# Kernel optimization log

Hardware: AMD Instinct MI355X
Metric: run time of the kernel (lower is better)

Reference implementation:

```python
import jax, jax.numpy as jnp
import numpy as np

EPS = 1e-5
MODES = 64
KERNEL = 25
PRED = 336
N_ENC = 2

def rmsnorm(x, w):
    return x * jax.lax.rsqrt(jnp.mean(jnp.square(x), axis=-1, keepdims=True) + EPS) * w

def ffn(x, w1, b1, w2, b2):
    return jax.nn.gelu(x @ w1 + b1, approximate=False) @ w2 + b2

def series_decomp(x):
    # moving average with zero padding (Conv1d, kernel=KERNEL, weight=1/KERNEL)
    pad = (KERNEL - 1) // 2
    xp = jnp.pad(x, ((0, 0), (pad, pad), (0, 0)))
    cs = jnp.cumsum(xp, axis=1)
    cs = jnp.concatenate([jnp.zeros_like(cs[:, :1]), cs], axis=1)
    t = (cs[:, KERNEL:, :] - cs[:, :-KERNEL, :]) / KERNEL  # [B,T,C]
    return x - t, t

def fourier_block(x, w, nw):
    # x: [B,T,C]; w: [MODES,C,2] learned complex weights; nw: [C] rms scale
    B, T, C = x.shape
    Xf = jnp.fft.rfft(x, axis=1)                      # [B,F,C] complex64
    mag = jnp.sum(Xf[:, 1:].real**2 + Xf[:, 1:].imag**2, axis=-1)  # [B,F-1]
    K = min(MODES, Xf.shape[1] - 1)
    _, idx = jax.lax.top_k(mag, K)
    idx = idx + 1                                      # skip DC, [B,K]
    Xsel = jnp.take_along_axis(Xf, idx[:, :, None], axis=1)  # [B,K,C]
    Wc = w[:K, :, 0] + 1j * w[:K, :, 1]               # [K,C]
    Ysel = Xsel * Wc[None]                             # [B,K,C]
    Yf = jnp.zeros_like(Xf).at[jnp.arange(B)[:, None], idx].set(Ysel)
    y = jnp.fft.irfft(Yf, n=T, axis=1)                 # [B,T,C]
    return rmsnorm(y, nw)

def setup_inputs() -> dict:
    key = jax.random.key(0)
    ks = iter(jax.random.split(key, 64))
    B, L, Cin, Cout, D, FF = 32, 1024, 8, 8, 512, 2048
    r = lambda *s: jax.random.normal(next(ks), s, dtype=jnp.float32) * 0.02
    z = lambda *s: jnp.zeros(s, dtype=jnp.float32)
    o = lambda *s: jnp.ones(s, dtype=jnp.float32)
    return {
        'x': jax.random.normal(next(ks), (B, L, Cin), dtype=jnp.float32),
        'enc_in_w': r(Cin, D), 'enc_in_b': z(D),
        'dec_in_w': r(Cin, D), 'dec_in_b': z(D),
        'enc_freq_w': r(N_ENC, MODES, D, 2), 'enc_freq_nw': o(N_ENC, D),
        'enc_n1': o(N_ENC, D), 'enc_n2': o(N_ENC, D),
        'enc_w1': r(N_ENC, D, FF), 'enc_b1': z(N_ENC, FF),
        'enc_w2': r(N_ENC, FF, D), 'enc_b2': z(N_ENC, D),
        'dec_freq_w': r(MODES, D, 2), 'dec_freq_nw': o(D),
        'dec_n1': o(D), 'dec_n2': o(D), 'dec_nx': o(D),
        'dec_cross_w': r(D, D), 'dec_cross_b': z(D),
        'dec_w1': r(D, FF), 'dec_b1': z(FF),
        'dec_w2': r(FF, D), 'dec_b2': z(D),
        'seas_w': r(D, Cout), 'seas_b': z(Cout),
        'tr_w1': r(D, FF), 'tr_b1': z(FF),
        'tr_w2': r(FF, Cout), 'tr_b2': z(Cout),
        'mix_w': r(Cout, Cout), 'mix_b': z(Cout),
        'qpos': jax.random.normal(next(ks), (1, PRED, D), dtype=jnp.float32) * 0.02,
    }

def reference(x, enc_in_w, enc_in_b, dec_in_w, dec_in_b,
              enc_freq_w, enc_freq_nw, enc_n1, enc_n2, enc_w1, enc_b1, enc_w2, enc_b2,
              dec_freq_w, dec_freq_nw, dec_n1, dec_n2, dec_nx, dec_cross_w, dec_cross_b,
              dec_w1, dec_b1, dec_w2, dec_b2, seas_w, seas_b,
              tr_w1, tr_b1, tr_w2, tr_b2, mix_w, mix_b, qpos):
    s, t = series_decomp(x)
    sez = s @ enc_in_w + enc_in_b                      # [B,L,D]
    for i in range(N_ENC):
        sez = sez + fourier_block(rmsnorm(sez, enc_n1[i]), enc_freq_w[i], enc_freq_nw[i])
        sez = sez + ffn(rmsnorm(sez, enc_n2[i]), enc_w1[i], enc_b1[i], enc_w2[i], enc_b2[i])
    memory = sez
    tgt = qpos + sez[:, -1:, :]                        # [B,PRED,D]
    # decoder layer
    m = jnp.mean(memory, axis=1, keepdims=True)        # [B,1,D]
    m = rmsnorm(m, dec_nx) @ dec_cross_w + dec_cross_b
    y = fourier_block(rmsnorm(tgt, dec_n1), dec_freq_w, dec_freq_nw)
    xd = tgt + y * jax.nn.sigmoid(m)
    xd = xd + ffn(rmsnorm(xd, dec_n2), dec_w1, dec_b1, dec_w2, dec_b2)
    sez_out = xd @ seas_w + seas_b                     # [B,PRED,Cout]
    tr = t @ dec_in_w + dec_in_b
    tr_out = ffn(tr[:, -1:, :], tr_w1, tr_b1, tr_w2, tr_b2)  # [B,1,Cout], broadcasts
    out = sez_out + tr_out
    return out @ mix_w + mix_b
```

## Files before the change

### kernel.cpp

```cpp
#include <hip/hip_runtime.h>
#include <hip/hip_fp16.h>
#include <math.h>

#define B_    32
#define L_    1024
#define D_    512
#define FF_   2048
#define PRED_ 336
#define ME_   (B_*L_)
#define MD_   (B_*PRED_)
#define EPS_  1e-5f

typedef _Float16 f16;
typedef _Float16 f16x8 __attribute__((ext_vector_type(8)));
typedef float    f32x4 __attribute__((ext_vector_type(4)));

__device__ __forceinline__ float wred64(float v) {
#pragma unroll
  for (int o = 32; o > 0; o >>= 1) v += __shfl_xor(v, o, 64);
  return v;
}
__device__ __forceinline__ double dwred64(double v) {
#pragma unroll
  for (int o = 32; o > 0; o >>= 1) v += __shfl_xor(v, o, 64);
  return v;
}
__device__ __forceinline__ float gelu_f(float x) {
  return 0.5f * x * (1.0f + erff(x * 0.7071067811865476f));
}
__device__ __forceinline__ void gl2lds16(const void* g, void* l) {
  __builtin_amdgcn_global_load_lds((const __attribute__((address_space(1))) void*)g,
                                   (__attribute__((address_space(3))) void*)l, 16, 0, 0);
}

__global__ void k_transpose_cast(const float* __restrict__ in, f16* __restrict__ out, int R, int C) {
  __shared__ float t[32][33];
  int c0 = blockIdx.x * 32, r0 = blockIdx.y * 32;
  int tx = threadIdx.x, ty = threadIdx.y;
#pragma unroll
  for (int j = ty; j < 32; j += 8) t[j][tx] = in[(size_t)(r0 + j) * C + c0 + tx];
  __syncthreads();
#pragma unroll
  for (int j = ty; j < 32; j += 8) out[(size_t)(c0 + j) * R + r0 + tx] = (f16)t[tx][j];
}

__global__ __launch_bounds__(256) void k_decomp_proj(const float* __restrict__ x,
    const float* __restrict__ w, const float* __restrict__ bias, float* __restrict__ sez) {
  int b = blockIdx.x, t0 = blockIdx.y * 128, tid = threadIdx.x;
  __shared__ float xs[152][8];
  __shared__ float st[128][8];
  __shared__ float wsm[8 * 512];
  __shared__ float bs[512];
  for (int i = tid; i < 152 * 8; i += 256) {
    int tt = i >> 3, c = i & 7; int tg = t0 - 12 + tt;
    xs[tt][c] = (tg >= 0 && tg < 1024) ? x[((size_t)b * 1024 + tg) * 8 + c] : 0.0f;
  }
  for (int i = tid; i < 4096; i += 256) wsm[i] = w[i];
  for (int i = tid; i < 512; i += 256) bs[i] = bias[i];
  __syncthreads();
  for (int i = tid; i < 1024; i += 256) {
    int t = i >> 3, c = i & 7;
    float s = 0.f;
#pragma unroll
    for (int j = 0; j < 25; ++j) s += xs[t + j][c];
    st[t][c] = xs[t + 12][c] - s / 25.0f;
  }
  __syncthreads();
#pragma unroll
  for (int g = 0; g < 2; ++g) {
    int d = tid + g * 256;
    float wb[8];
#pragma unroll
    for (int c = 0; c < 8; ++c) wb[c] = wsm[c * 512 + d];
    float bb = bs[d];
    for (int t = 0; t < 128; ++t) {
      float o = bb;
#pragma unroll
      for (int c = 0; c < 8; ++c) o += st[t][c] * wb[c];
      sez[((size_t)b * 1024 + t0 + t) * 512 + d] = o;
    }
  }
}

__global__ __launch_bounds__(512) void k_trend_trin(const float* __restrict__ x, const float* __restrict__ w,
    const float* __restrict__ bias, float* __restrict__ trin) {
  int b = blockIdx.x, tid = threadIdx.x;
  __shared__ float tl[8];
  if (tid < 8) {
    float s = 0.f;
    for (int j = 1011; j <= 1023; ++j) s += x[((size_t)b * 1024 + j) * 8 + tid];
    tl[tid] = s / 25.0f;
  }
  __syncthreads();
  float acc = bias[tid];
#pragma unroll
  for (int c = 0; c < 8; ++c) acc += tl[c] * w[c * 512 + tid];
  trin[b * 512 + tid] = acc;
}

__global__ __launch_bounds__(256) void k_rinv(const float* __restrict__ xin, float* __restrict__ rinv) {
  int row = blockIdx.x * 4 + (threadIdx.x >> 6), lane = threadIdx.x & 63;
  const float4* p = (const float4*)(xin + (size_t)row * 512);
  float4 a = p[lane * 2], b = p[lane * 2 + 1];
  float ss = a.x*a.x + a.y*a.y + a.z*a.z + a.w*a.w + b.x*b.x + b.y*b.y + b.z*b.z + b.w*b.w;
  ss = wred64(ss);
  if (lane == 0) rinv[row] = rsqrtf(ss * (1.0f / 512.0f) + EPS_);
}

__global__ __launch_bounds__(256) void k_rms_f16(const float* __restrict__ xin, const float* __restrict__ w,
    f16* __restrict__ out) {
  int row = blockIdx.x * 4 + (threadIdx.x >> 6), lane = threadIdx.x & 63;
  const float4* p = (const float4*)(xin + (size_t)row * 512);
  float4 a = p[lane * 2], b = p[lane * 2 + 1];
  float ss = a.x*a.x + a.y*a.y + a.z*a.z + a.w*a.w + b.x*b.x + b.y*b.y + b.z*b.z + b.w*b.w;
  ss = wred64(ss);
  float ri = rsqrtf(ss * (1.0f / 512.0f) + EPS_);
  const float4* wp = (const float4*)w;
  float4 wa = wp[lane * 2], wb = wp[lane * 2 + 1];
  float va[8] = {a.x, a.y, a.z, a.w, b.x, b.y, b.z, b.w};
  float wv[8] = {wa.x, wa.y, wa.z, wa.w, wb.x, wb.y, wb.z, wb.w};
  f16x8 o;
#pragma unroll
  for (int j = 0; j < 8; ++j) o[j] = (f16)((va[j] * ri) * wv[j]);
  *(f16x8*)(out + (size_t)row * 512 + lane * 8) = o;
}

#define IDX_(i) ((i) + ((i) >> 4))
__global__ __launch_bounds__(256) void k_fft_enc(const float* __restrict__ sez, const float* __restrict__ rinv,
    const float* __restrict__ n1, float* __restrict__ Xf) {
  int b = blockIdx.x, c0 = blockIdx.y * 4, tid = threadIdx.x;
  __shared__ double Zr[2][1088], Zi[2][1088];
  __shared__ double TWr[256], TWi[256];
  if (tid < 256) {
    double a = -6.283185307179586232 * (double)tid / 1024.0;
    TWr[tid] = cos(a); TWi[tid] = sin(a);
  }
  for (int i = tid; i < 4096; i += 256) {
    int t = i >> 2, cl = i & 3;
    float xv = (sez[((size_t)b * 1024 + t) * 512 + c0 + cl] * rinv[b * 1024 + t]) * n1[c0 + cl];
    int u = t, rt = 0;
#pragma unroll
    for (int d = 0; d < 5; ++d) { rt = (rt << 2) | (u & 3); u >>= 2; }
    if (cl & 1) Zi[cl >> 1][IDX_(rt)] = (double)xv; else Zr[cl >> 1][IDX_(rt)] = (double)xv;
  }
  __syncthreads();
#pragma unroll
  for (int s = 0; s < 5; ++s) {
    const int lh = 2 * s, h = 1 << lh;
#pragma unroll
    for (int qi = 0; qi < 2; ++qi) {
      int q = tid + qi * 256;
      int p = q >> 8, qq = q & 255;
      int j = qq & (h - 1), g = qq >> lh;
      int p0 = (g << (lh + 2)) + j;
      int i0 = IDX_(p0), i1 = IDX_(p0 + h), i2 = IDX_(p0 + 2 * h), i3 = IDX_(p0 + 3 * h);
      int tw = j << (8 - lh);
      double w1r = TWr[tw], w1i = TWi[tw];
      double w2r = w1r * w1r - w1i * w1i, w2i = 2.0 * w1r * w1i;
      double w3r = w2r * w1r - w2i * w1i, w3i = w2r * w1i + w2i * w1r;
      double Ar = Zr[p][i0], Ai = Zi[p][i0];
      double br = Zr[p][i1], bi = Zi[p][i1];
      double cr = Zr[p][i2], ci = Zi[p][i2];
      double dr = Zr[p][i3], di = Zi[p][i3];
      double Br = br * w1r - bi * w1i, Bi = br * w1i + bi * w1r;
      double Cr = cr * w2r - ci * w2i, Ci = cr * w2i + ci * w2r;
      double Dr = dr * w3r - di * w3i, Di = dr * w3i + di * w3r;
      double T0r = Ar + Cr, T0i = Ai + Ci;
      double T1r = Ar - Cr, T1i = Ai - Ci;
      double T2r = Br + Dr, T2i = Bi + Di;
      double T3r = Bi - Di, T3i = Dr - Br;
      Zr[p][i0] = T0r + T2r; Zi[p][i0] = T0i + T2i;
      Zr[p][i1] = T1r + T3r; Zi[p][i1] = T1i + T3i;
      Zr[p][i2] = T0r - T2r; Zi[p][i2] = T0i - T2i;
      Zr[p][i3] = T1r - T3r; Zi[p][i3] = T1i - T3i;
    }
    __syncthreads();
  }
  for (int i = tid; i < 513 * 2; i += 256) {
    int f = i >> 1, p = i & 1;
    int mf = (1024 - f) & 1023;
    double Ar = Zr[p][IDX_(f)], Ai = Zi[p][IDX_(f)], Br = Zr[p][IDX_(mf)], Bi = Zi[p][IDX_(mf)];
    float4 o;
    o.x = (float)(0.5 * (Ar + Br)); o.y = (float)(0.5 * (Ai - Bi));
    o.z = (float)(0.5 * (Ai + Bi)); o.w = (float)(0.5 * (Br - Ar));
    *(float4*)&Xf[(((size_t)b * 513 + f) * 512 + c0 + 2 * p) * 2] = o;
  }
}

__global__ __launch_bounds__(256) void k_mag(const float* __restrict__ Xf, double* __restrict__ mag, int F) {
  int b = blockIdx.x, f = blockIdx.y + 1, tid = threadIdx.x;
  const float2* row = (const float2*)(Xf + ((size_t)b * F + f) * 512 * 2);
  double s = 0;
  for (int c = tid; c < 512; c += 256) { float2 v = row[c]; s += (double)v.x * v.x + (double)v.y * v.y; }
  s = dwred64(s);
  __shared__ double ps[4];
  if ((tid & 63) == 0) ps[tid >> 6] = s;
  __syncthreads();
  if (tid == 0) mag[b * 513 + f] = ps[0] + ps[1] + ps[2] + ps[3];
}

__global__ __launch_bounds__(256) void k_topk(const double* __restrict__ mag, int* __restrict__ idx, int F) {
  int b = blockIdx.x, tid = threadIdx.x;
  __shared__ double v[528];
  __shared__ double rv[256];
  __shared__ int ri[256];
  for (int s = tid; s < 528; s += 256) v[s] = (s >= 1 && s < F) ? mag[b * 513 + s] : -1e300;
  __syncthreads();
  for (int r = 0; r < 64; ++r) {
    double bv = -1e300; int bi = 0;
    for (int s = tid; s < 528; s += 256) { double xv = v[s]; if (xv > bv) { bv = xv; bi = s; } }
    rv[tid] = bv; ri[tid] = bi;
    __syncthreads();
    for (int st = 128; st > 0; st >>= 1) {
      if (tid < st) {
        double o = rv[tid + st]; int oi = ri[tid + st];
        if (o > rv[tid] || (o == rv[tid] && oi < ri[tid])) { rv[tid] = o; ri[tid] = oi; }
      }
      __syncthreads();
    }
    if (tid == 0) { idx[b * 64 + r] = ri[0]; v[ri[0]] = -1e300; }
    __syncthreads();
  }
}

__global__ __launch_bounds__(512) void k_gather(const float* __restrict__ Xf, const int* __restrict__ idx,
    const float* __restrict__ fw, float* __restrict__ Ysel, int F, int T) {
  int b = blockIdx.x, k = blockIdx.y, c = threadIdx.x;
  int f = idx[b * 64 + k];
  float sc = (2 * f == T) ? (1.0f / (float)T) : (2.0f / (float)T);
  float2 xv = *(const float2*)&Xf[(((size_t)b * F + f) * 512 + c) * 2];
  float wr = fw[(k * 512 + c) * 2], wi = fw[(k * 512 + c) * 2 + 1];
  float yr = (xv.x * wr - xv.y * wi) * sc;
  float yi = (xv.x * wi + xv.y * wr) * sc;
  *(float2*)&Ysel[((size_t)(b * 64 + k) * 512 + c) * 2] = make_float2(yr, yi);
}

template <int T>
__global__ __launch_bounds__(256) void k_irfft(const float* __restrict__ Ysel, const int* __restrict__ idx,
    const float* __restrict__ nw, const float* __restrict__ sig,
    float* __restrict__ dst, int mode) {
  int b = blockIdx.x, t0 = blockIdx.y * 16, tid = threadIdx.x;
  int cq = tid & 127;
  int tg = tid >> 7;
  __shared__ float tcT[16][68], tsT[16][68];
  __shared__ int sidx[64];
  __shared__ float red[4][8];
  __shared__ float rfac[16];
  if (tid < 64) sidx[tid] = idx[b * 64 + tid];
  __syncthreads();
  for (int i = tid; i < 1024; i += 256) {
    int k = i >> 4, tt = i & 15;
    int m = (sidx[k] * (t0 + tt)) % T;
    float ang = (float)m * (float)(6.283185307179586232 / (double)T);
    tcT[tt][k] = cosf(ang);
    tsT[tt][k] = sinf(ang);
  }
  __syncthreads();
  float acc[8][4];
#pragma unroll
  for (int q = 0; q < 8; ++q)
#pragma unroll
    for (int j = 0; j < 4; ++j) acc[q][j] = 0.f;
  const float4* ys = (const float4*)Ysel + (size_t)b * 64 * 256 + 2 * cq;
  for (int k4 = 0; k4 < 64; k4 += 4) {
    float4 ya[4], yb[4];
#pragma unroll
    for (int kk = 0; kk < 4; ++kk) {
      ya[kk] = ys[(size_t)(k4 + kk) * 256];
      yb[kk] = ys[(size_t)(k4 + kk) * 256 + 1];
    }
#pragma unroll
    for (int q = 0; q < 8; ++q) {
      int tt = tg * 8 + q;
      float4 c4 = *(const float4*)&tcT[tt][k4];
      float4 s4 = *(const float4*)&tsT[tt][k4];
      acc[q][0] += ya[0].x * c4.x - ya[0].y * s4.x;
      acc[q][1] += ya[0].z * c4.x - ya[0].w * s4.x;
      acc[q][2] += yb[0].x * c4.x - yb[0].y * s4.x;
      acc[q][3] += yb[0].z * c4.x - yb[0].w * s4.x;
      acc[q][0] += ya[1].x * c4.y - ya[1].y * s4.y;
      acc[q][1] += ya[1].z * c4.y - ya[1].w * s4.y;
      acc[q][2] += yb[1].x * c4.y - yb[1].y * s4.y;
      acc[q][3] += yb[1].z * c4.y - yb[1].w * s4.y;
      acc[q][0] += ya[2].x * c4.z - ya[2].y * s4.z;
      acc[q][1] += ya[2].z * c4.z - ya[2].w * s4.z;
      acc[q][2] += yb[2].x * c4.z - yb[2].y * s4.z;
      acc[q][3] += yb[2].z * c4.z - yb[2].w * s4.z;
      acc[q][0] += ya[3].x * c4.w - ya[3].y * s4.w;
      acc[q][1] += ya[3].z * c4.w - ya[3].w * s4.w;
      acc[q][2] += yb[3].x * c4.w - yb[3].y * s4.w;
      acc[q][3] += yb[3].z * c4.w - yb[3].w * s4.w;
    }
  }
  int lane = tid & 63, wv = tid >> 6;
#pragma unroll
  for (int q = 0; q < 8; ++q) {
    float v = wred64(acc[q][0] * acc[q][0] + acc[q][1] * acc[q][1]
                   + acc[q][2] * acc[q][2] + acc[q][3] * acc[q][3]);
    if (lane == 0) red[wv][q] = v;
  }
  __syncthreads();
  if (tid < 16) {
    int tg2 = tid >> 3, q = tid & 7;
    float s = red[tg2 * 2][q] + red[tg2 * 2 + 1][q];
    rfac[tid] = rsqrtf(s * (1.0f / 512.0f) + EPS_);
  }
  __syncthreads();
  int c = 4 * cq;
  float4 wc = *(const float4*)&nw[c];
  float4 sg = (mode == 1) ? *(const float4*)&sig[b * 512 + c] : make_float4(1.f, 1.f, 1.f, 1.f);
  float* drow = dst + ((size_t)b * T + t0) * 512 + c;
#pragma unroll
  for (int q = 0; q < 8; ++q) {
    int tt = tg * 8 + q;
    float rf = rfac[tt];
    float4 cur = *(float4*)&drow[(size_t)tt * 512];
    float y0 = (acc[q][0] * rf) * wc.x;
    float y1 = (acc[q][1] * rf) * wc.y;
    float y2 = (acc[q][2] * rf) * wc.z;
    float y3 = (acc[q][3] * rf) * wc.w;
    cur.x += (mode == 1) ? y0 * sg.x : y0;
    cur.y += (mode == 1) ? y1 * sg.y : y1;
    cur.z += (mode == 1) ? y2 * sg.z : y2;
    cur.w += (mode == 1) ? y3 * sg.w : y3;
    *(float4*)&drow[(size_t)tt * 512] = cur;
  }
}

template <int MODE>
__global__ __launch_bounds__(256) void k_gemm(const f16* __restrict__ A, const f16* __restrict__ Bt,
    const float* __restrict__ bias, float* __restrict__ Cf, f16* __restrict__ Ch,
    int M, int N, int K, int nbn) {
  __shared__ f16 lA[128][64];
  __shared__ f16 lB[128][64];
  int nwg = gridDim.x;
  int q8 = nwg >> 3;
  int wgid = (blockIdx.x & 7) * q8 + (blockIdx.x >> 3);
  int bm = wgid / nbn, bn = wgid - bm * nbn;
  int tid = threadIdx.x, lane = tid & 63, w = tid >> 6;
  int wr = w >> 1, wcq = w & 1;
  f32x4 acc[4][4];
#pragma unroll
  for (int i = 0; i < 4; ++i)
#pragma unroll
    for (int j = 0; j < 4; ++j) acc[i][j] = (f32x4){0.f, 0.f, 0.f, 0.f};
  int lr = lane >> 3;
  int kk = (lane & 7) * 8;
  int nk = K >> 6;
  for (int kt = 0; kt < nk; ++kt) {
    __syncthreads();
#pragma unroll
    for (int i = 0; i < 4; ++i) {
      int rt = (w * 4 + i) * 8;
      int rr = rt + lr;
      gl2lds16(A + (size_t)(bm * 128 + rr) * K + kt * 64 + kk, &lA[rt][0]);
      gl2lds16(Bt + (size_t)(bn * 128 + rr) * K + kt * 64 + kk, &lB[rt][0]);
    }
    __syncthreads();
#pragma unroll
    for (int ki = 0; ki < 2; ++ki) {
      f16x8 af[4], bf[4];
#pragma unroll
      for (int mi = 0; mi < 4; ++mi)
        af[mi] = *(const f16x8*)&lA[wr * 64 + mi * 16 + (lane & 15)][ki * 32 + (lane >> 4) * 8];
#pragma unroll
      for (int ni = 0; ni < 4; ++ni)
        bf[ni] = *(const f16x8*)&lB[wcq * 64 + ni * 16 + (lane & 15)][ki * 32 + (lane >> 4) * 8];
#pragma unroll
      for (int mi = 0; mi < 4; ++mi)
#pragma unroll
        for (int ni = 0; ni < 4; ++ni)
          acc[mi][ni] = __builtin_amdgcn_mfma_f32_16x16x32_f16(af[mi], bf[ni], acc[mi][ni], 0, 0, 0);
    }
  }
  int cbase = bn * 128 + wcq * 64;
  int rbase = bm * 128 + wr * 64;
#pragma unroll
  for (int mi = 0; mi < 4; ++mi)
#pragma unroll
    for (int ni = 0; ni < 4; ++ni) {
      int cg = cbase + ni * 16 + (lane & 15);
      float bv = bias[cg];
#pragma unroll
      for (int q = 0; q < 4; ++q) {
        int rg = rbase + mi * 16 + (lane >> 4) * 4 + q;
        float val = acc[mi][ni][q] + bv;
        if (MODE == 0) Ch[(size_t)rg * N + cg] = (f16)gelu_f(val);
        else           Cf[(size_t)rg * N + cg] += val;
      }
    }
}

__global__ __launch_bounds__(256) void k_mc_part(const float* __restrict__ sez, float* __restrict__ mcp) {
  int b = blockIdx.x, ch = blockIdx.y, tid = threadIdx.x;
  for (int d = tid; d < 512; d += 256) {
    float s = 0.f;
    for (int t = 0; t < 128; ++t) s += sez[((size_t)b * 1024 + ch * 128 + t) * 512 + d];
    mcp[((size_t)b * 8 + ch) * 512 + d] = s;
  }
}
__global__ __launch_bounds__(512) void k_mc_fin(const float* __restrict__ mcp, const float* __restrict__ nx,
    const float* __restrict__ Wc, const float* __restrict__ cb, float* __restrict__ sig) {
  int b = blockIdx.x, d = threadIdx.x;
  float m = 0.f;
#pragma unroll
  for (int ch = 0; ch < 8; ++ch) m += mcp[((size_t)b * 8 + ch) * 512 + d];
  m *= (1.0f / 1024.0f);
  float ss = wred64(m * m);
  __shared__ float ps[8];
  __shared__ float mn[512];
  int lane = d & 63, wv = d >> 6;
  if (lane == 0) ps[wv] = ss;
  __syncthreads();
  float tot = 0.f;
#pragma unroll
  for (int i = 0; i < 8; ++i) tot += ps[i];
  float ri = rsqrtf(tot * (1.0f / 512.0f) + EPS_);
  mn[d] = (m * ri) * nx[d];
  __syncthreads();
  float accv = cb[d];
  for (int e = 0; e < 512; ++e) accv += mn[e] * Wc[(size_t)e * 512 + d];
  sig[b * 512 + d] = 1.0f / (1.0f + expf(-accv));
}

__global__ __launch_bounds__(512) void k_make_tgt(const float* __restrict__ sez, const float* __restrict__ qpos,
    const float* __restrict__ n1, float* __restrict__ tgt, float* __restrict__ tgt_n,
    float* __restrict__ rinvd) {
  int row = blockIdx.x, d = threadIdx.x;
  int b = row / 336, p = row % 336;
  float v = qpos[(size_t)p * 512 + d] + sez[((size_t)b * 1024 + 1023) * 512 + d];
  tgt[(size_t)row * 512 + d] = v;
  float ss = wred64(v * v);
  __shared__ float ps[8];
  if ((d & 63) == 0) ps[d >> 6] = ss;
  __syncthreads();
  float t = 0.f;
#pragma unroll
  for (int i = 0; i < 8; ++i) t += ps[i];
  float ri = rsqrtf(t * (1.0f / 512.0f) + EPS_);
  tgt_n[(size_t)row * 512 + d] = (v * ri) * n1[d];
  if (d == 0) rinvd[row] = ri;
}

__global__ void k_dtab(double* __restrict__ dtt) {
  int f = blockIdx.x;
  for (int t = threadIdx.x; t < 336; t += 256) {
    double cv = 0.0, sv = 0.0;
    if (f < 169) {
      int m = (f * t) % 336;
      double a = 6.283185307179586232 * (double)m / 336.0;
      cv = cos(a); sv = sin(a);
    }
    dtt[((size_t)t * 176 + f) * 2]     = cv;
    dtt[((size_t)t * 176 + f) * 2 + 1] = sv;
  }
}
__global__ __launch_bounds__(512) void k_dft_dec(const float* __restrict__ tgt_n,
    const double* __restrict__ dtt, float* __restrict__ Xf) {
  int b = blockIdx.x, f0 = blockIdx.y * 4, c = threadIdx.x;
  double ar[4], ai[4];
#pragma unroll
  for (int i = 0; i < 4; ++i) { ar[i] = 0.0; ai[i] = 0.0; }
  const float* trow = tgt_n + (size_t)b * 336 * 512 + c;
  for (int t = 0; t < 336; ++t) {
    double xd = (double)trow[(size_t)t * 512];
    const double* tab = dtt + ((size_t)t * 176 + f0) * 2;
#pragma unroll
    for (int ff = 0; ff < 4; ++ff) {
      ar[ff] += xd * tab[ff * 2];
      ai[ff] -= xd * tab[ff * 2 + 1];
    }
  }
#pragma unroll
  for (int ff = 0; ff < 4; ++ff) {
    int f = f0 + ff;
    if (f < 169)
      *(float2*)&Xf[(((size_t)b * 169 + f) * 512 + c) * 2] = make_float2((float)ar[ff], (float)ai[ff]);
  }
}

__global__ __launch_bounds__(256) void k_tr_h(const float* __restrict__ trin, const float* __restrict__ w1,
    const float* __restrict__ b1, float* __restrict__ H) {
  int b = blockIdx.x, j0 = blockIdx.y * 512, tid = threadIdx.x;
  __shared__ float xs[512];
  for (int i = tid; i < 512; i += 256) xs[i] = trin[b * 512 + i];
  __syncthreads();
  int j = j0 + tid;
  float h0 = b1[j], h1 = b1[j + 256];
  const float* wp = w1 + j;
#pragma unroll 4
  for (int e = 0; e < 512; ++e) {
    float xe = xs[e];
    h0 += xe * wp[(size_t)e * 2048];
    h1 += xe * wp[(size_t)e * 2048 + 256];
  }
  H[b * 2048 + j] = gelu_f(h0);
  H[b * 2048 + j + 256] = gelu_f(h1);
}

__global__ __launch_bounds__(256) void k_tr_red(const float* __restrict__ H, const float* __restrict__ w2,
    const float* __restrict__ b2, float* __restrict__ trout) {
  int b = blockIdx.x, tid = threadIdx.x;
  __shared__ float red[4][8];
  float part[8];
#pragma unroll
  for (int co = 0; co < 8; ++co) part[co] = 0.f;
#pragma unroll
  for (int jj = 0; jj < 8; ++jj) {
    int j = tid + jj * 256;
    float g = H[b * 2048 + j];
    float4 wa = *(const float4*)&w2[(size_t)j * 8];
    float4 wb = *(const float4*)&w2[(size_t)j * 8 + 4];
    part[0] += g * wa.x; part[1] += g * wa.y; part[2] += g * wa.z; part[3] += g * wa.w;
    part[4] += g * wb.x; part[5] += g * wb.y; part[6] += g * wb.z; part[7] += g * wb.w;
  }
  int lane = tid & 63, wv = tid >> 6;
#pragma unroll
  for (int co = 0; co < 8; ++co) {
    float v = wred64(part[co]);
    if (lane == 0) red[wv][co] = v;
  }
  __syncthreads();
  if (tid < 8) trout[b * 8 + tid] = red[0][tid] + red[1][tid] + red[2][tid] + red[3][tid] + b2[tid];
}

__global__ __launch_bounds__(256) void k_head(const float* __restrict__ xd, const float* __restrict__ sw,
    const float* __restrict__ sb, const float* __restrict__ trout, const float* __restrict__ mw,
    const float* __restrict__ mb, float* __restrict__ outp) {
  int row = blockIdx.x, tid = threadIdx.x;
  int b = row / 336;
  __shared__ float wsm[512 * 8];
  __shared__ float red[4][8];
  __shared__ float srow[8];
  for (int i = tid; i < 4096; i += 256) wsm[i] = sw[i];
  __syncthreads();
  float part[8];
#pragma unroll
  for (int co = 0; co < 8; ++co) part[co] = 0.f;
#pragma unroll
  for (int g = 0; g < 2; ++g) {
    int d = tid + g * 256;
    float xv = xd[(size_t)row * 512 + d];
#pragma unroll
    for (int co = 0; co < 8; ++co) part[co] += xv * wsm[d * 8 + co];
  }
  int lane = tid & 63, wv = tid >> 6;
#pragma unroll
  for (int co = 0; co < 8; ++co) {
    float v = wred64(part[co]);
    if (lane == 0) red[wv][co] = v;
  }
  __syncthreads();
  if (tid == 0) {
#pragma unroll
    for (int co = 0; co < 8; ++co)
      srow[co] = red[0][co] + red[1][co] + red[2][co] + red[3][co] + sb[co] + trout[b * 8 + co];
  }
  __syncthreads();
  if (tid < 8) {
    float o = mb[tid];
#pragma unroll
    for (int co = 0; co < 8; ++co) o += srow[co] * mw[co * 8 + tid];
    outp[(size_t)row * 8 + tid] = o;
  }
}

extern "C" void kernel_launch(void* const* d_in, const int* in_sizes, int n_in,
                              void* d_out, int out_size, void* d_ws, size_t ws_size,
                              hipStream_t stream) {
  const float* x        = (const float*)d_in[0];
  const float* enc_in_w = (const float*)d_in[1];
  const float* enc_in_b = (const float*)d_in[2];
  const float* dec_in_w = (const float*)d_in[3];
  const float* dec_in_b = (const float*)d_in[4];
  const float* enc_fw   = (const float*)d_in[5];
  const float* enc_fnw  = (const float*)d_in[6];
  const float* enc_n1   = (const float*)d_in[7];
  const float* enc_n2   = (const float*)d_in[8];
  const float* enc_w1   = (const float*)d_in[9];
  const float* enc_b1   = (const float*)d_in[10];
  const float* enc_w2   = (const float*)d_in[11];
  const float* enc_b2   = (const float*)d_in[12];
  const float* dec_fw   = (const float*)d_in[13];
  const float* dec_fnw  = (const float*)d_in[14];
  const float* dec_n1   = (const float*)d_in[15];
  const float* dec_n2   = (const float*)d_in[16];
  const float* dec_nx   = (const float*)d_in[17];
  const float* dec_cw   = (const float*)d_in[18];
  const float* dec_cb   = (const float*)d_in[19];
  const float* dec_w1   = (const float*)d_in[20];
  const float* dec_b1   = (const float*)d_in[21];
  const float* dec_w2   = (const float*)d_in[22];
  const float* dec_b2   = (const float*)d_in[23];
  const float* seas_w   = (const float*)d_in[24];
  const float* seas_b   = (const float*)d_in[25];
  const float* tr_w1    = (const float*)d_in[26];
  const float* tr_b1    = (const float*)d_in[27];
  const float* tr_w2    = (const float*)d_in[28];
  const float* tr_b2    = (const float*)d_in[29];
  const float* mix_w    = (const float*)d_in[30];
  const float* mix_b    = (const float*)d_in[31];
  const float* qpos     = (const float*)d_in[32];
  float* outp = (float*)d_out;
  (void)in_sizes; (void)n_in; (void)out_size; (void)ws_size;

  char* wsb = (char*)d_ws;
  size_t off = 0;
  auto take = [&](size_t n) -> char* {
    char* p = wsb + off;
    off = (off + n + 255) & ~(size_t)255;
    return p;
  };
  float*  sez   = (float*)take((size_t)ME_ * 512 * 4);
  f16*    xn    = (f16*)take((size_t)ME_ * 512 * 2);
  const size_t XF_BYTES = (size_t)32 * 513 * 512 * 2 * 4;
  char*   arena = take(XF_BYTES + (size_t)32 * 64 * 512 * 2 * 4);
  float*  Xf    = (float*)arena;
  f16*    hbuf  = (f16*)arena;
  float*  Ysel  = (float*)(arena + XF_BYTES);
  float*  tgt   = (float*)take((size_t)MD_ * 512 * 4);
  float*  tgt_n = (float*)take((size_t)MD_ * 512 * 4);
  double* mag   = (double*)take((size_t)32 * 513 * 8);
  int*    idx   = (int*)take((size_t)32 * 64 * 4);
  float*  rinvp = (float*)take((size_t)ME_ * 4);
  float*  rinvd = (float*)take((size_t)MD_ * 4);
  float*  mcp   = (float*)take((size_t)32 * 8 * 512 * 4);
  float*  sig   = (float*)take((size_t)32 * 512 * 4);
  float*  trin  = (float*)take((size_t)32 * 512 * 4);
  float*  trout = (float*)take((size_t)32 * 8 * 4);
  float*  trH   = (float*)take((size_t)32 * 2048 * 4);
  double* dtt   = (double*)take((size_t)336 * 176 * 2 * 8);
  f16*    w1t   = (f16*)take((size_t)2 * 2048 * 512 * 2);
  f16*    w2t   = (f16*)take((size_t)2 * 512 * 2048 * 2);
  f16*    dw1t  = (f16*)take((size_t)2048 * 512 * 2);
  f16*    dw2t  = (f16*)take((size_t)512 * 2048 * 2);

  k_transpose_cast<<<dim3(64, 16), dim3(32, 8), 0, stream>>>(enc_w1, w1t, 512, 2048);
  k_transpose_cast<<<dim3(64, 16), dim3(32, 8), 0, stream>>>(enc_w1 + 512 * 2048, w1t + 2048 * 512, 512, 2048);
  k_transpose_cast<<<dim3(16, 64), dim3(32, 8), 0, stream>>>(enc_w2, w2t, 2048, 512);
  k_transpose_cast<<<dim3(16, 64), dim3(32, 8), 0, stream>>>(enc_w2 + 2048 * 512, w2t + 512 * 2048, 2048, 512);
  k_transpose_cast<<<dim3(64, 16), dim3(32, 8), 0, stream>>>(dec_w1, dw1t, 512, 2048);
  k_transpose_cast<<<dim3(16, 64), dim3(32, 8), 0, stream>>>(dec_w2, dw2t, 2048, 512);

  k_decomp_proj<<<dim3(32, 8), 256, 0, stream>>>(x, enc_in_w, enc_in_b, sez);
  k_trend_trin<<<32, 512, 0, stream>>>(x, dec_in_w, dec_in_b, trin);

  k_tr_h<<<dim3(32, 4), 256, 0, stream>>>(trin, tr_w1, tr_b1, trH);
  k_tr_red<<<32, 256, 0, stream>>>(trH, tr_w2, tr_b2, trout);

  for (int i = 0; i < 2; ++i) {
    k_rinv<<<ME_ / 4, 256, 0, stream>>>(sez, rinvp);
    k_fft_enc<<<dim3(32, 128), 256, 0, stream>>>(sez, rinvp, enc_n1 + i * 512, Xf);
    k_mag<<<dim3(32, 512), 256, 0, stream>>>(Xf, mag, 513);
    k_topk<<<32, 256, 0, stream>>>(mag, idx, 513);
    k_gather<<<dim3(32, 64), 512, 0, stream>>>(Xf, idx, enc_fw + (size_t)i * 64 * 512 * 2, Ysel, 513, 1024);
    k_irfft<1024><<<dim3(32, 64), 256, 0, stream>>>(Ysel, idx, enc_fnw + i * 512, nullptr, sez, 0);
    k_rms_f16<<<ME_ / 4, 256, 0, stream>>>(sez, enc_n2 + i * 512, xn);
    for (int ck = 0; ck < 2; ++ck) {
      const f16* Ax = xn + (size_t)ck * 16384 * 512;
      float* Cx = sez + (size_t)ck * 16384 * 512;
      k_gemm<0><<<128 * 16, 256, 0, stream>>>(Ax, w1t + (size_t)i * 2048 * 512, enc_b1 + i * 2048,
                                              nullptr, hbuf, 16384, 2048, 512, 16);
      k_gemm<1><<<128 * 4, 256, 0, stream>>>(hbuf, w2t + (size_t)i * 512 * 2048, enc_b2 + i * 512,
                                             Cx, nullptr, 16384, 512, 2048, 4);
    }
  }

  k_mc_part<<<dim3(32, 8), 256, 0, stream>>>(sez, mcp);
  k_mc_fin<<<32, 512, 0, stream>>>(mcp, dec_nx, dec_cw, dec_cb, sig);
  k_make_tgt<<<MD_, 512, 0, stream>>>(sez, qpos, dec_n1, tgt, tgt_n, rinvd);
  k_dtab<<<176, 256, 0, stream>>>(dtt);
  k_dft_dec<<<dim3(32, 43), 512, 0, stream>>>(tgt_n, dtt, Xf);
  k_mag<<<dim3(32, 168), 256, 0, stream>>>(Xf, mag, 169);
  k_topk<<<32, 256, 0, stream>>>(mag, idx, 169);
  k_gather<<<dim3(32, 64), 512, 0, stream>>>(Xf, idx, dec_fw, Ysel, 169, 336);
  k_irfft<336><<<dim3(32, 21), 256, 0, stream>>>(Ysel, idx, dec_fnw, sig, tgt, 1);
  k_rms_f16<<<MD_ / 4, 256, 0, stream>>>(tgt, dec_n2, xn);
  k_gemm<0><<<84 * 16, 256, 0, stream>>>(xn, dw1t, dec_b1, nullptr, hbuf, MD_, 2048, 512, 16);
  k_gemm<1><<<84 * 4, 256, 0, stream>>>(hbuf, dw2t, dec_b2, tgt, nullptr, MD_, 512, 2048, 4);

  k_head<<<MD_, 256, 0, stream>>>(tgt, seas_w, seas_b, trout, mix_w, mix_b, outp);
}
```

Measured before the change: 1.640 ms.

## Double-buffer LDS in FFN GEMM and drop XCD block remapping

The FFN GEMM now keeps two LDS buffers, issuing the global-to-LDS loads for the next K tile before computing on the current one, with explicit vmcnt waits and barriers. This is meant to hide global load latency behind the MFMA work. It also removes the XCD-aware workgroup index remapping and uses a 2D grid, which may change L2 locality across chiplets. LDS use per block doubles to 64KB, which may lower occupancy.

After: 1.578 ms. 3.8% less time.

```diff
diff --git a/kernel.cpp b/kernel.cpp
--- a/kernel.cpp
+++ b/kernel.cpp
@@ -330,13 +330,10 @@
 template <int MODE>
 __global__ __launch_bounds__(256) void k_gemm(const f16* __restrict__ A, const f16* __restrict__ Bt,
     const float* __restrict__ bias, float* __restrict__ Cf, f16* __restrict__ Ch,
-    int M, int N, int K, int nbn) {
-  __shared__ f16 lA[128][64];
-  __shared__ f16 lB[128][64];
-  int nwg = gridDim.x;
-  int q8 = nwg >> 3;
-  int wgid = (blockIdx.x & 7) * q8 + (blockIdx.x >> 3);
-  int bm = wgid / nbn, bn = wgid - bm * nbn;
+    int M, int N, int K) {
+  __shared__ f16 lA[2][128][64];
+  __shared__ f16 lB[2][128][64];
+  int bm = blockIdx.x, bn = blockIdx.y;
   int tid = threadIdx.x, lane = tid & 63, w = tid >> 6;
   int wr = w >> 1, wcq = w & 1;
   f32x4 acc[4][4];
@@ -347,31 +344,41 @@
   int lr = lane >> 3;
   int kk = (lane & 7) * 8;
   int nk = K >> 6;
-  for (int kt = 0; kt < nk; ++kt) {
-    __syncthreads();
+  auto STAGE = [&](int buf, int kt) {
 #pragma unroll
     for (int i = 0; i < 4; ++i) {
       int rt = (w * 4 + i) * 8;
       int rr = rt + lr;
-      gl2lds16(A + (size_t)(bm * 128 + rr) * K + kt * 64 + kk, &lA[rt][0]);
-      gl2lds16(Bt + (size_t)(bn * 128 + rr) * K + kt * 64 + kk, &lB[rt][0]);
-    }
-    __syncthreads();
+      gl2lds16(A + (size_t)(bm * 128 + rr) * K + kt * 64 + kk, &lA[buf][rt][0]);
+      gl2lds16(Bt + (size_t)(bn * 128 + rr) * K + kt * 64 + kk, &lB[buf][rt][0]);
+    }
+  };
+  STAGE(0, 0);
+  int cur = 0;
+  for (int kt = 0; kt < nk; ++kt) {
+    if (kt + 1 < nk) {
+      STAGE(cur ^ 1, kt + 1);
+      asm volatile("s_waitcnt vmcnt(8)\n\ts_barrier" ::: "memory");
+    } else {
+      asm volatile("s_waitcnt vmcnt(0)\n\ts_barrier" ::: "memory");
+    }
 #pragma unroll
     for (int ki = 0; ki < 2; ++ki) {
       f16x8 af[4], bf[4];
 #pragma unroll
       for (int mi = 0; mi < 4; ++mi)
-        af[mi] = *(const f16x8*)&lA[wr * 64 + mi * 16 + (lane & 15)][ki * 32 + (lane >> 4) * 8];
+        af[mi] = *(const f16x8*)&lA[cur][wr * 64 + mi * 16 + (lane & 15)][ki * 32 + (lane >> 4) * 8];
 #pragma unroll
       for (int ni = 0; ni < 4; ++ni)
-        bf[ni] = *(const f16x8*)&lB[wcq * 64 + ni * 16 + (lane & 15)][ki * 32 + (lane >> 4) * 8];
+        bf[ni] = *(const f16x8*)&lB[cur][wcq * 64 + ni * 16 + (lane & 15)][ki * 32 + (lane >> 4) * 8];
 #pragma unroll
       for (int mi = 0; mi < 4; ++mi)
 #pragma unroll
         for (int ni = 0; ni < 4; ++ni)
           acc[mi][ni] = __builtin_amdgcn_mfma_f32_16x16x32_f16(af[mi], bf[ni], acc[mi][ni], 0, 0, 0);
     }
+    asm volatile("s_barrier" ::: "memory");
+    cur ^= 1;
   }
   int cbase = bn * 128 + wcq * 64;
   int rbase = bm * 128 + wr * 64;
@@ -659,10 +666,10 @@
     for (int ck = 0; ck < 2; ++ck) {
       const f16* Ax = xn + (size_t)ck * 16384 * 512;
       float* Cx = sez + (size_t)ck * 16384 * 512;
-      k_gemm<0><<<128 * 16, 256, 0, stream>>>(Ax, w1t + (size_t)i * 2048 * 512, enc_b1 + i * 2048,
-                                              nullptr, hbuf, 16384, 2048, 512, 16);
-      k_gemm<1><<<128 * 4, 256, 0, stream>>>(hbuf, w2t + (size_t)i * 512 * 2048, enc_b2 + i * 512,
-                                             Cx, nullptr, 16384, 512, 2048, 4);
+      k_gemm<0><<<dim3(128, 16), 256, 0, stream>>>(Ax, w1t + (size_t)i * 2048 * 512, enc_b1 + i * 2048,
+                                                   nullptr, hbuf, 16384, 2048, 512);
+      k_gemm<1><<<dim3(128, 4), 256, 0, stream>>>(hbuf, w2t + (size_t)i * 512 * 2048, enc_b2 + i * 512,
+                                                  Cx, nullptr, 16384, 512, 2048);
     }
   }
 
@@ -676,8 +683,8 @@
   k_gather<<<dim3(32, 64), 512, 0, stream>>>(Xf, idx, dec_fw, Ysel, 169, 336);
   k_irfft<336><<<dim3(32, 21), 256, 0, stream>>>(Ysel, idx, dec_fnw, sig, tgt, 1);
   k_rms_f16<<<MD_ / 4, 256, 0, stream>>>(tgt, dec_n2, xn);
-  k_gemm<0><<<84 * 16, 256, 0, stream>>>(xn, dw1t, dec_b1, nullptr, hbuf, MD_, 2048, 512, 16);
-  k_gemm<1><<<84 * 4, 256, 0, stream>>>(hbuf, dw2t, dec_b2, tgt, nullptr, MD_, 512, 2048, 4);
+  k_gemm<0><<<dim3(84, 16), 256, 0, stream>>>(xn, dw1t, dec_b1, nullptr, hbuf, MD_, 2048, 512);
+  k_gemm<1><<<dim3(84, 4), 256, 0, stream>>>(hbuf, dw2t, dec_b2, tgt, nullptr, MD_, 512, 2048);
 
   k_head<<<MD_, 256, 0, stream>>>(tgt, seas_w, seas_b, trout, mix_w, mix_b, outp);
 }
```
